# Performance work log

Hardware: AMD Instinct MI355X
Metric: run time of the kernel (lower is better)

Reference implementation:

```python
import math
import jax, jax.numpy as jnp
import numpy as np

N = 512; E_EDGES = 16384; NODE_DIM = 64; HID = 128; FF = 2048; VOCAB = 50; L = 2; H = 8; SEQ = 100


def setup_inputs() -> dict:
    key = jax.random.key(0)
    ks = jax.random.split(key, 24)
    s = 0.02
    rn = lambda k, shape: jax.random.normal(k, shape, jnp.float32) * s
    return {
        "x": jax.random.normal(ks[0], (N, NODE_DIM), jnp.float32),
        "edge_index": jax.random.randint(ks[1], (2, E_EDGES), 0, N, dtype=jnp.int32),
        "gcn1_w": rn(ks[2], (NODE_DIM, HID)), "gcn1_b": rn(ks[3], (HID,)),
        "gcn2_w": rn(ks[4], (HID, HID)),     "gcn2_b": rn(ks[5], (HID,)),
        "fc_w":   rn(ks[6], (HID, HID)),     "fc_b":   rn(ks[7], (HID,)),
        # decoder: per layer, 4 proj mats (q,k,v,out) for self-attn and cross-attn
        "sa_w": rn(ks[8], (L, 4, HID, HID)), "sa_b": rn(ks[9], (L, 4, HID)),
        "ca_w": rn(ks[10], (L, 4, HID, HID)), "ca_b": rn(ks[11], (L, 4, HID)),
        "ln_w": jnp.ones((L, 3, HID), jnp.float32), "ln_b": jnp.zeros((L, 3, HID), jnp.float32),
        "ff_w1": rn(ks[12], (L, HID, FF)), "ff_b1": rn(ks[13], (L, FF)),
        "ff_w2": rn(ks[14], (L, FF, HID)), "ff_b2": rn(ks[15], (L, HID)),
        "out_w": rn(ks[16], (HID, VOCAB)), "out_b": rn(ks[17], (VOCAB,)),
    }


def _gcn(x, W, b, src, dst, n):
    # PyG GCNConv: add self-loops, symmetric norm, aggregate source->target
    h = x @ W                                   # [N, out]
    loop = jnp.arange(n, dtype=src.dtype)
    s = jnp.concatenate([src, loop])
    d = jnp.concatenate([dst, loop])
    deg = jax.ops.segment_sum(jnp.ones_like(d, x.dtype), d, num_segments=n)
    dinv = jax.lax.rsqrt(deg)                   # deg >= 1 thanks to self-loops
    norm = dinv[s] * dinv[d]                    # [E+N]
    return jax.ops.segment_sum(h[s] * norm[:, None], d, num_segments=n) + b


def _layernorm(x, w, b, eps=1e-5):
    m = x.mean(-1, keepdims=True)
    v = ((x - m) ** 2).mean(-1, keepdims=True)
    return (x - m) * jax.lax.rsqrt(v + eps) * w + b


def _mha(q_in, kv_in, w, b):
    # q_in [S,Nb,E], kv_in [T,Nb,E]; w [4,E,E] (q,k,v,out), b [4,E]
    S, Nb, E = q_in.shape
    T = kv_in.shape[0]
    Dh = E // H
    q = (q_in @ w[0] + b[0]).reshape(S, Nb, H, Dh)
    k = (kv_in @ w[1] + b[1]).reshape(T, Nb, H, Dh)
    v = (kv_in @ w[2] + b[2]).reshape(T, Nb, H, Dh)
    att = jnp.einsum('snhd,tnhd->nhst', q, k) / math.sqrt(Dh)
    p = jax.nn.softmax(att, axis=-1)
    o = jnp.einsum('nhst,tnhd->snhd', p, v).reshape(S, Nb, E)
    return o @ w[3] + b[3]


def _forward(x, edge_index, gcn1_w, gcn1_b, gcn2_w, gcn2_b, fc_w, fc_b,
             sa_w, sa_b, ca_w, ca_b, ln_w, ln_b, ff_w1, ff_b1, ff_w2, ff_b2,
             out_w, out_b):
    n = x.shape[0]
    src, dst = edge_index[0], edge_index[1]
    # quantum_embedding: rz = (cos(phi)-sin(phi)) * (cos(theta)*x + sin(theta)*tanh(x))
    qx = (math.cos(0.05) - math.sin(0.05)) * (math.cos(0.1) * x + math.sin(0.1) * jnp.tanh(x))
    h = jax.nn.relu(_gcn(qx, gcn1_w, gcn1_b, src, dst, n))
    h = jax.nn.relu(_gcn(h, gcn2_w, gcn2_b, src, dst, n))
    h = h @ fc_w + fc_b                          # [N, HID]
    mem = h[None]                                # [1, N, HID] (memory, seq-first)
    tgt = jnp.zeros((SEQ, n, h.shape[1]), h.dtype)
    for l in range(L):                           # post-norm TransformerDecoderLayer
        tgt = _layernorm(tgt + _mha(tgt, tgt, sa_w[l], sa_b[l]), ln_w[l, 0], ln_b[l, 0])
        tgt = _layernorm(tgt + _mha(tgt, mem, ca_w[l], ca_b[l]), ln_w[l, 1], ln_b[l, 1])
        f = jax.nn.relu(tgt @ ff_w1[l] + ff_b1[l]) @ ff_w2[l] + ff_b2[l]
        tgt = _layernorm(tgt + f, ln_w[l, 2], ln_b[l, 2])
    return tgt @ out_w + out_b                   # [SEQ, N, VOCAB]


def reference(x, edge_index, gcn1_w, gcn1_b, gcn2_w, gcn2_b, fc_w, fc_b,
              sa_w, sa_b, ca_w, ca_b, ln_w, ln_b, ff_w1, ff_b1, ff_w2, ff_b2,
              out_w, out_b):
    return _forward(x, edge_index, gcn1_w, gcn1_b, gcn2_w, gcn2_b, fc_w, fc_b,
                    sa_w, sa_b, ca_w, ca_b, ln_w, ln_b, ff_w1, ff_b1, ff_w2, ff_b2,
                    out_w, out_b)
```

## Files before the change

### kernel.cpp

```cpp
#include <hip/hip_runtime.h>
#include <math.h>

#define NN      512
#define EE      16384
#define NDIM    64
#define HID     128
#define FFD     2048
#define VOCAB   50
#define SEQ     100

#define QA 0.94877109112428797f
#define QB 0.99500416527802582f
#define QC 0.099833416646828155f


__global__ void k_prep(const float* __restrict__ x, float* __restrict__ qx,
                       int* __restrict__ cnt) {
    int i = blockIdx.x * 256 + threadIdx.x;
    if (i < NN * NDIM) {
        float v = x[i];
        qx[i] = QA * (QB * v + QC * tanhf(v));
    }
    if (i < NN) cnt[i] = 0;
}


struct BArgs {
    const int* ei; int* cnt;
    const float* qx; const float* g1w; float* pre1;
    const float* A[3]; const float* ab[3]; const float* Bm[3]; const float* bb[3];
    float* outM[3];
    const float* ab3; const float* B3; const float* bb3; float* out3;
};

__global__ void k_b(BArgs a) {
    int B = blockIdx.x, t = threadIdx.x;
    if (B < 64) {
        int e = B * 256 + t;
        atomicAdd(&a.cnt[a.ei[EE + e]], 1);
        return;
    }
    if (B < 320) {
        int i = (B - 64) * 256 + t;
        int row = i >> 7, col = i & 127;
        const float* xr = a.qx + row * NDIM;
        float acc = 0.0f;
#pragma unroll 8
        for (int k = 0; k < NDIM; k++) acc = fmaf(xr[k], a.g1w[k * HID + col], acc);
        a.pre1[i] = acc;
        return;
    }
    if (B < 320 + 195) {
        int q = B - 320;
        int jm = q / 65;
        int i = (q - jm * 65) * 256 + t;
        if (i >= 129 * HID) return;
        int rw = i >> 7, col = i & 127;
        const float* Bm = a.Bm[jm];
        float acc;
        if (rw < 128) {
            const float* ar = a.A[jm] + rw * HID;
            acc = 0.0f;
#pragma unroll 8
            for (int k = 0; k < HID; k++) acc = fmaf(ar[k], Bm[k * HID + col], acc);
        } else {
            acc = a.bb[jm][col];
#pragma unroll 8
            for (int k = 0; k < HID; k++) acc = fmaf(a.ab[jm][k], Bm[k * HID + col], acc);
        }
        a.outM[jm][i] = acc;
        return;
    }
    if (t < HID) {
        float acc = a.bb3[t];
#pragma unroll 8
        for (int k = 0; k < HID; k++) acc = fmaf(a.ab3[k], a.B3[k * HID + t], acc);
        a.out3[t] = acc;
    }
}


struct CArgs {
    const int* cnt; int* offs; int* cursor; float* dinv;
    const float* fcw; const float* fcb;
    const float* Mca0; const float* Mca1; float* Mfc0; float* Mfc1;
};

__global__ void k_c(CArgs a) {
    int B = blockIdx.x, t = threadIdx.x;
    if (B == 0) {
        __shared__ int sh[512];
        int c0 = a.cnt[t], c1 = a.cnt[t + 256];
        sh[t] = c0; sh[t + 256] = c1;
        __syncthreads();
        for (int o = 1; o < 512; o <<= 1) {
            int x0 = (t >= o) ? sh[t - o] : 0;
            int x1 = (t + 256 >= o) ? sh[t + 256 - o] : 0;
            __syncthreads();
            sh[t] += x0; sh[t + 256] += x1;
            __syncthreads();
        }
        a.offs[t + 1] = sh[t];
        a.offs[t + 257] = sh[t + 256];
        if (t == 0) a.offs[0] = 0;
        a.cursor[t] = sh[t] - c0;
        a.cursor[t + 256] = sh[t + 256] - c1;
        a.dinv[t] = rsqrtf((float)c0 + 1.0f);
        a.dinv[t + 256] = rsqrtf((float)c1 + 1.0f);
        return;
    }
    int q = B - 1;
    int jm = q / 65;
    int i = (q - jm * 65) * 256 + t;
    if (i >= 129 * HID) return;
    int rw = i >> 7, col = i & 127;
    const float* M = jm ? a.Mca1 : a.Mca0;
    float* o = jm ? a.Mfc1 : a.Mfc0;
    float acc;
    if (rw < 128) {
        const float* ar = a.fcw + rw * HID;
        acc = 0.0f;
#pragma unroll 8
        for (int k = 0; k < HID; k++) acc = fmaf(ar[k], M[k * HID + col], acc);
    } else {
        acc = M[128 * HID + col];
#pragma unroll 8
        for (int k = 0; k < HID; k++) acc = fmaf(a.fcb[k], M[k * HID + col], acc);
    }
    o[i] = acc;
}


__global__ void k_scatter(const int* __restrict__ ei, int* __restrict__ cursor,
                          int* __restrict__ csr) {
    int e = blockIdx.x * 256 + threadIdx.x;
    if (e < EE) {
        int d = ei[EE + e];
        int slot = atomicAdd(&cursor[d], 1);
        csr[slot] = ei[e];
    }
}


__device__ __forceinline__ float gather_row(const float* __restrict__ pre,
                                            const float* __restrict__ dinv,
                                            const int* __restrict__ offs,
                                            const int* __restrict__ csr,
                                            int row, int j) {
    float dd = dinv[row];
    float acc = pre[row * HID + j] * dd;
    int i = offs[row], e = offs[row + 1];
    for (; i + 3 < e; i += 4) {
        int s0 = csr[i], s1 = csr[i + 1], s2 = csr[i + 2], s3 = csr[i + 3];
        float a0 = pre[s0 * HID + j] * dinv[s0];
        float a1 = pre[s1 * HID + j] * dinv[s1];
        float a2 = pre[s2 * HID + j] * dinv[s2];
        float a3 = pre[s3 * HID + j] * dinv[s3];
        acc += (a0 + a1) + (a2 + a3);
    }
    for (; i < e; ++i) {
        int s = csr[i];
        acc += pre[s * HID + j] * dinv[s];
    }
    return acc * dd;
}

__device__ __forceinline__ float rowln(float v, float w, float b, float* sh, int t) {
    int r = t >> 7;
    float s1 = v, s2 = v * v;
#pragma unroll
    for (int o = 32; o > 0; o >>= 1) {
        s1 += __shfl_down(s1, o);
        s2 += __shfl_down(s2, o);
    }
    int wv = (t >> 6) & 1;
    if ((t & 63) == 0) { sh[r * 4 + wv] = s1; sh[r * 4 + 2 + wv] = s2; }
    __syncthreads();
    float mean = (sh[r * 4] + sh[r * 4 + 1]) * (1.0f / HID);
    float m2   = (sh[r * 4 + 2] + sh[r * 4 + 3]) * (1.0f / HID);
    float rstd = rsqrtf(m2 - mean * mean + 1e-5f);
    float out = (v - mean) * rstd * w + b;
    __syncthreads();
    return out;
}


__global__ void k_gather_mm(const float* __restrict__ pre1, const float* __restrict__ dinv,
                            const int* __restrict__ offs, const int* __restrict__ csr,
                            const float* __restrict__ g1b, const float* __restrict__ g2w,
                            float* __restrict__ pre2) {
    __shared__ float sh_h[2][HID];
    int t = threadIdx.x, j = t & 127, r = t >> 7;
    int row = blockIdx.x * 2 + r;
    float g = gather_row(pre1, dinv, offs, csr, row, j);
    sh_h[r][j] = fmaxf(g + g1b[j], 0.0f);
    __syncthreads();
    float acc = 0.0f;
#pragma unroll 8
    for (int k = 0; k < HID; k++) acc = fmaf(sh_h[r][k], g2w[k * HID + j], acc);
    pre2[row * HID + j] = acc;
}


__global__ void k_row0(const float* __restrict__ pre2, const float* __restrict__ dinv,
                       const int* __restrict__ offs, const int* __restrict__ csr,
                       const float* __restrict__ g2b,
                       const float* __restrict__ Mfc0, const float* __restrict__ Mfc1,
                       const float* __restrict__ sa0bias,
                       const float* __restrict__ ln0w, const float* __restrict__ ln0b,
                       const float* __restrict__ ln1w, const float* __restrict__ ln1b,
                       float* __restrict__ ca1out, float* __restrict__ t0out) {
    __shared__ float sh_h[2][HID];
    __shared__ float shln[8];
    int t = threadIdx.x, j = t & 127, r = t >> 7;
    int row = blockIdx.x * 2 + r;
    float g = gather_row(pre2, dinv, offs, csr, row, j);
    sh_h[r][j] = fmaxf(g + g2b[j], 0.0f);
    __syncthreads();
    float a0 = Mfc0[128 * HID + j], a1 = Mfc1[128 * HID + j];
#pragma unroll 4
    for (int k = 0; k < HID; k++) {
        float hk = sh_h[r][k];
        a0 = fmaf(hk, Mfc0[k * HID + j], a0);
        a1 = fmaf(hk, Mfc1[k * HID + j], a1);
    }
    ca1out[row * HID + j] = a1;
    float v = rowln(sa0bias[j], ln0w[j], ln0b[j], shln, t);
    v = rowln(v + a0, ln1w[j], ln1b[j], shln, t);
    t0out[row * HID + j] = v;
}


__global__ void k_fff(const float* __restrict__ tin, const float* __restrict__ W1,
                      const float* __restrict__ b1, const float* __restrict__ W2,
                      float* __restrict__ part) {
    __shared__ float sh_t[8][HID];
    __shared__ float sh_m[8][256];
    int t = threadIdx.x;
    int kc = blockIdx.x & 7, rg = blockIdx.x >> 3;
    int row0 = rg * 8, c0 = kc * 256;
#pragma unroll
    for (int q = 0; q < 4; q++) {
        int i = q * 256 + t;
        sh_t[i >> 7][i & 127] = tin[row0 * HID + i];
    }
    __syncthreads();
    float acc[8];
    float bias = b1[c0 + t];
#pragma unroll
    for (int r = 0; r < 8; r++) acc[r] = bias;
#pragma unroll 4
    for (int k = 0; k < HID; k++) {
        float w = W1[k * FFD + c0 + t];
#pragma unroll
        for (int r = 0; r < 8; r++) acc[r] = fmaf(sh_t[r][k], w, acc[r]);
    }
#pragma unroll
    for (int r = 0; r < 8; r++) sh_m[r][t] = fmaxf(acc[r], 0.0f);
    __syncthreads();
    int col = t & 127, rr0 = (t >> 7) * 4;
    float a2[4] = {0.f, 0.f, 0.f, 0.f};
#pragma unroll 4
    for (int kk = 0; kk < 256; kk++) {
        float w = W2[(c0 + kk) * HID + col];
#pragma unroll
        for (int q = 0; q < 4; q++) a2[q] = fmaf(sh_m[rr0 + q][kk], w, a2[q]);
    }
#pragma unroll
    for (int q = 0; q < 4; q++)
        part[kc * (NN * HID) + (row0 + rr0 + q) * HID + col] = a2[q];
}


__global__ void k_row1(const float* __restrict__ part, const float* __restrict__ fb2,
                       const float* __restrict__ t0, const float* __restrict__ Msa1,
                       const float* __restrict__ ca1,
                       const float* __restrict__ ln2w, const float* __restrict__ ln2b,
                       const float* __restrict__ ln3w, const float* __restrict__ ln3b,
                       const float* __restrict__ ln4w, const float* __restrict__ ln4b,
                       float* __restrict__ t2out) {
    __shared__ float sh_t1[2][HID];
    __shared__ float shln[8];
    int t = threadIdx.x, j = t & 127, r = t >> 7;
    int row = blockIdx.x * 2 + r;
    float v = fb2[j] + t0[row * HID + j];
#pragma unroll
    for (int s = 0; s < 8; s++) v += part[s * (NN * HID) + row * HID + j];
    v = rowln(v, ln2w[j], ln2b[j], shln, t);
    sh_t1[r][j] = v;
    __syncthreads();
    float s1 = Msa1[128 * HID + j];
#pragma unroll 8
    for (int k = 0; k < HID; k++) s1 = fmaf(sh_t1[r][k], Msa1[k * HID + j], s1);
    float u = rowln(v + s1, ln3w[j], ln3b[j], shln, t);
    u = rowln(u + ca1[row * HID + j], ln4w[j], ln4b[j], shln, t);
    t2out[row * HID + j] = u;
}


__global__ void k_rowout(const float* __restrict__ part, const float* __restrict__ fb2,
                         const float* __restrict__ t2,
                         const float* __restrict__ ln5w, const float* __restrict__ ln5b,
                         const float* __restrict__ ow, const float* __restrict__ ob,
                         float* __restrict__ out) {
    __shared__ float sh3[2][HID];
    __shared__ float shln[8];
    __shared__ float sh_lg[100];
    int t = threadIdx.x, j = t & 127, r = t >> 7;
    int row = blockIdx.x * 2 + r;
    float v = fb2[j] + t2[row * HID + j];
#pragma unroll
    for (int s = 0; s < 8; s++) v += part[s * (NN * HID) + row * HID + j];
    v = rowln(v, ln5w[j], ln5b[j], shln, t);
    sh3[r][j] = v;
    __syncthreads();
    if (j < VOCAB) {
        float acc = ob[j];
#pragma unroll 8
        for (int k = 0; k < HID; k++) acc = fmaf(sh3[r][k], ow[k * VOCAB + j], acc);
        sh_lg[r * VOCAB + j] = acc;
    }
    __syncthreads();
    int base = blockIdx.x * (2 * VOCAB);
    for (int idx = t; idx < SEQ * 2 * VOCAB; idx += 256) {
        int s = idx / (2 * VOCAB), p = idx - s * (2 * VOCAB);
        out[s * (NN * VOCAB) + base + p] = sh_lg[p];
    }
}


extern "C" void kernel_launch(void* const* d_in, const int* in_sizes, int n_in,
                              void* d_out, int out_size, void* d_ws, size_t ws_size,
                              hipStream_t stream) {
    (void)in_sizes; (void)n_in; (void)out_size; (void)ws_size;
    const float* x   = (const float*)d_in[0];
    const int*   ei  = (const int*)d_in[1];
    const float* g1w = (const float*)d_in[2];
    const float* g1b = (const float*)d_in[3];
    const float* g2w = (const float*)d_in[4];
    const float* g2b = (const float*)d_in[5];
    const float* fcw = (const float*)d_in[6];
    const float* fcb = (const float*)d_in[7];
    const float* saw = (const float*)d_in[8];
    const float* sab = (const float*)d_in[9];
    const float* caw = (const float*)d_in[10];
    const float* cab = (const float*)d_in[11];
    const float* lnw = (const float*)d_in[12];
    const float* lnb = (const float*)d_in[13];
    const float* fw1 = (const float*)d_in[14];
    const float* fb1 = (const float*)d_in[15];
    const float* fw2 = (const float*)d_in[16];
    const float* fb2 = (const float*)d_in[17];
    const float* ow  = (const float*)d_in[18];
    const float* ob  = (const float*)d_in[19];
    float* out = (float*)d_out;

    float* ws      = (float*)d_ws;
    float* qx      = ws;
    float* pre1    = ws + 32768;
    float* pre2    = ws + 98304;
    float* t0      = ws + 163840;
    float* t2      = ws + 229376;
    float* ca1     = ws + 294912;
    float* Msa1    = ws + 360448;
    float* Mca0    = ws + 376960;
    float* Mca1    = ws + 393472;
    float* Mfc0    = ws + 409984;
    float* Mfc1    = ws + 426496;
    float* sa0bias = ws + 443008;
    float* dinv    = ws + 443136;
    int*   cnt     = (int*)(ws + 443648);
    int*   offs    = cnt + 512;
    int*   cursor  = offs + 516;
    int*   csr     = cursor + 512;
    float* part    = ws + 461824;

    k_prep<<<128, 256, 0, stream>>>(x, qx, cnt);

    {
        BArgs a;
        a.ei = ei; a.cnt = cnt; a.qx = qx; a.g1w = g1w; a.pre1 = pre1;
        a.A[0]  = saw + (4 + 2) * HID * HID;  a.ab[0] = sab + (4 + 2) * HID;
        a.Bm[0] = saw + (4 + 3) * HID * HID;  a.bb[0] = sab + (4 + 3) * HID;
        a.outM[0] = Msa1;
        a.A[1]  = caw + 2 * HID * HID;        a.ab[1] = cab + 2 * HID;
        a.Bm[1] = caw + 3 * HID * HID;        a.bb[1] = cab + 3 * HID;
        a.outM[1] = Mca0;
        a.A[2]  = caw + (4 + 2) * HID * HID;  a.ab[2] = cab + (4 + 2) * HID;
        a.Bm[2] = caw + (4 + 3) * HID * HID;  a.bb[2] = cab + (4 + 3) * HID;
        a.outM[2] = Mca1;
        a.ab3 = sab + 2 * HID;  a.B3 = saw + 3 * HID * HID;  a.bb3 = sab + 3 * HID;
        a.out3 = sa0bias;
        k_b<<<516, 256, 0, stream>>>(a);
    }

    {
        CArgs a;
        a.cnt = cnt; a.offs = offs; a.cursor = cursor; a.dinv = dinv;
        a.fcw = fcw; a.fcb = fcb;
        a.Mca0 = Mca0; a.Mca1 = Mca1; a.Mfc0 = Mfc0; a.Mfc1 = Mfc1;
        k_c<<<131, 256, 0, stream>>>(a);
    }

    k_scatter<<<64, 256, 0, stream>>>(ei, cursor, csr);

    k_gather_mm<<<256, 256, 0, stream>>>(pre1, dinv, offs, csr, g1b, g2w, pre2);

    k_row0<<<256, 256, 0, stream>>>(pre2, dinv, offs, csr, g2b, Mfc0, Mfc1, sa0bias,
                                    lnw + 0 * HID, lnb + 0 * HID,
                                    lnw + 1 * HID, lnb + 1 * HID, ca1, t0);

    k_fff<<<512, 256, 0, stream>>>(t0, fw1, fb1, fw2, part);

    k_row1<<<256, 256, 0, stream>>>(part, fb2, t0, Msa1, ca1,
                                    lnw + 2 * HID, lnb + 2 * HID,
                                    lnw + 3 * HID, lnb + 3 * HID,
                                    lnw + 4 * HID, lnb + 4 * HID, t2);

    k_fff<<<512, 256, 0, stream>>>(t2, fw1 + HID * FFD, fb1 + FFD, fw2 + FFD * HID, part);

    k_rowout<<<256, 256, 0, stream>>>(part, fb2 + HID, t2,
                                      lnw + 5 * HID, lnb + 5 * HID, ow, ob, out);
}
```

Measured before the change: 113.4 us.

## Prefetch FFN weights into cache in k_b and vectorize k_fff with 512 threads

Adds 512 extra blocks to k_b that read the FFN weight matrices fw1/fw2 and write a dummy reduction, so the weights are warm in L2/MALL by the time k_fff runs. k_fff is rewritten to use 512 threads with float4 weight loads, each thread computing 4 columns per row. The second GEMM is split over two halves of K and reduced through shared memory. This costs extra traffic and blocks in k_b and a dummy workspace output, plus an added shared-memory reduction step.

```diff
diff --git a/kernel.cpp b/kernel.cpp
--- a/kernel.cpp
+++ b/kernel.cpp
@@ -31,6 +31,7 @@
     const float* A[3]; const float* ab[3]; const float* Bm[3]; const float* bb[3];
     float* outM[3];
     const float* ab3; const float* B3; const float* bb3; float* out3;
+    const float* fw1; const float* fw2; float* pf;
 };
 
 __global__ void k_b(BArgs a) {
@@ -71,11 +72,25 @@
         a.outM[jm][i] = acc;
         return;
     }
-    if (t < HID) {
-        float acc = a.bb3[t];
-#pragma unroll 8
-        for (int k = 0; k < HID; k++) acc = fmaf(a.ab3[k], a.B3[k * HID + t], acc);
-        a.out3[t] = acc;
+    if (B == 515) {
+        if (t < HID) {
+            float acc = a.bb3[t];
+#pragma unroll 8
+            for (int k = 0; k < HID; k++) acc = fmaf(a.ab3[k], a.B3[k * HID + t], acc);
+            a.out3[t] = acc;
+        }
+        return;
+    }
+    {
+        int q = B - 516;
+        const float4* p = (const float4*)((q < 256) ? (a.fw1 + q * 2048)
+                                                    : (a.fw2 + (q - 256) * 2048));
+        float4 f0 = p[t];
+        float4 f1 = p[t + 256];
+        float s = (f0.x + f0.y + f0.z + f0.w) + (f1.x + f1.y + f1.z + f1.w);
+#pragma unroll
+        for (int o = 32; o > 0; o >>= 1) s += __shfl_down(s, o);
+        if ((t & 63) == 0) a.pf[q * 4 + (t >> 6)] = s;
     }
 }
 
@@ -231,44 +246,71 @@
 }
 
 
-__global__ void k_fff(const float* __restrict__ tin, const float* __restrict__ W1,
-                      const float* __restrict__ b1, const float* __restrict__ W2,
-                      float* __restrict__ part) {
+__global__ __launch_bounds__(512, 4)
+void k_fff(const float* __restrict__ tin, const float* __restrict__ W1,
+           const float* __restrict__ b1, const float* __restrict__ W2,
+           float* __restrict__ part) {
     __shared__ float sh_t[8][HID];
     __shared__ float sh_m[8][256];
     int t = threadIdx.x;
     int kc = blockIdx.x & 7, rg = blockIdx.x >> 3;
     int row0 = rg * 8, c0 = kc * 256;
-#pragma unroll
-    for (int q = 0; q < 4; q++) {
-        int i = q * 256 + t;
-        sh_t[i >> 7][i & 127] = tin[row0 * HID + i];
-    }
-    __syncthreads();
-    float acc[8];
-    float bias = b1[c0 + t];
-#pragma unroll
-    for (int r = 0; r < 8; r++) acc[r] = bias;
-#pragma unroll 4
-    for (int k = 0; k < HID; k++) {
-        float w = W1[k * FFD + c0 + t];
-#pragma unroll
-        for (int r = 0; r < 8; r++) acc[r] = fmaf(sh_t[r][k], w, acc[r]);
-    }
-#pragma unroll
-    for (int r = 0; r < 8; r++) sh_m[r][t] = fmaxf(acc[r], 0.0f);
-    __syncthreads();
-    int col = t & 127, rr0 = (t >> 7) * 4;
-    float a2[4] = {0.f, 0.f, 0.f, 0.f};
-#pragma unroll 4
-    for (int kk = 0; kk < 256; kk++) {
-        float w = W2[(c0 + kk) * HID + col];
-#pragma unroll
-        for (int q = 0; q < 4; q++) a2[q] = fmaf(sh_m[rr0 + q][kk], w, a2[q]);
-    }
-#pragma unroll
-    for (int q = 0; q < 4; q++)
-        part[kc * (NN * HID) + (row0 + rr0 + q) * HID + col] = a2[q];
+
+    if (t < 256) {
+        const float4* tp = (const float4*)(tin + row0 * HID);
+        float4 v = tp[t];
+        *(float4*)&sh_t[t >> 5][(t & 31) * 4] = v;
+    }
+    __syncthreads();
+
+    {
+        int rowg = t >> 6;
+        int col4 = (t & 63) * 4;
+        float4 bias = *(const float4*)&b1[c0 + col4];
+        float a0 = bias.x, a1 = bias.y, a2 = bias.z, a3 = bias.w;
+        const float* w1p = W1 + c0 + col4;
+#pragma unroll 8
+        for (int k = 0; k < HID; k++) {
+            float4 w = *(const float4*)&w1p[k * FFD];
+            float s = sh_t[rowg][k];
+            a0 = fmaf(s, w.x, a0); a1 = fmaf(s, w.y, a1);
+            a2 = fmaf(s, w.z, a2); a3 = fmaf(s, w.w, a3);
+        }
+        float4 m;
+        m.x = fmaxf(a0, 0.f); m.y = fmaxf(a1, 0.f);
+        m.z = fmaxf(a2, 0.f); m.w = fmaxf(a3, 0.f);
+        *(float4*)&sh_m[rowg][col4] = m;
+    }
+    __syncthreads();
+
+    {
+        int col4 = (t & 31) * 4;
+        int rowg = (t >> 5) & 7;
+        int half = t >> 8;
+        int kb = half * 128;
+        float a0 = 0.f, a1 = 0.f, a2 = 0.f, a3 = 0.f;
+        const float* w2p = W2 + (c0 + kb) * HID + col4;
+        const float* mp = &sh_m[rowg][kb];
+#pragma unroll 8
+        for (int kk = 0; kk < 128; kk++) {
+            float4 w = *(const float4*)&w2p[kk * HID];
+            float m = mp[kk];
+            a0 = fmaf(m, w.x, a0); a1 = fmaf(m, w.y, a1);
+            a2 = fmaf(m, w.z, a2); a3 = fmaf(m, w.w, a3);
+        }
+        __syncthreads();
+        float* shred = &sh_t[0][0];
+        if (half) {
+            float4 r; r.x = a0; r.y = a1; r.z = a2; r.w = a3;
+            *(float4*)&shred[(t - 256) * 4] = r;
+        }
+        __syncthreads();
+        if (!half) {
+            float4 o = *(float4*)&shred[t * 4];
+            o.x += a0; o.y += a1; o.z += a2; o.w += a3;
+            *(float4*)&part[kc * (NN * HID) + (row0 + rowg) * HID + col4] = o;
+        }
+    }
 }
 
 
@@ -374,6 +416,7 @@
     int*   cursor  = offs + 516;
     int*   csr     = cursor + 512;
     float* part    = ws + 461824;
+    float* pf      = ws + 986112;
 
     k_prep<<<128, 256, 0, stream>>>(x, qx, cnt);
 
@@ -391,7 +434,8 @@
         a.outM[2] = Mca1;
         a.ab3 = sab + 2 * HID;  a.B3 = saw + 3 * HID * HID;  a.bb3 = sab + 3 * HID;
         a.out3 = sa0bias;
-        k_b<<<516, 256, 0, stream>>>(a);
+        a.fw1 = fw1; a.fw2 = fw2; a.pf = pf;
+        k_b<<<1028, 256, 0, stream>>>(a);
     }
 
     {
@@ -410,14 +454,14 @@
                                     lnw + 0 * HID, lnb + 0 * HID,
                                     lnw + 1 * HID, lnb + 1 * HID, ca1, t0);
 
-    k_fff<<<512, 256, 0, stream>>>(t0, fw1, fb1, fw2, part);
+    k_fff<<<512, 512, 0, stream>>>(t0, fw1, fb1, fw2, part);
 
     k_row1<<<256, 256, 0, stream>>>(part, fb2, t0, Msa1, ca1,
                                     lnw + 2 * HID, lnb + 2 * HID,
                                     lnw + 3 * HID, lnb + 3 * HID,
                                     lnw + 4 * HID, lnb + 4 * HID, t2);
 
-    k_fff<<<512, 256, 0, stream>>>(t2, fw1 + HID * FFD, fb1 + FFD, fw2 + FFD * HID, part);
+    k_fff<<<512, 512, 0, stream>>>(t2, fw1 + HID * FFD, fb1 + FFD, fw2 + FFD * HID, part);
 
     k_rowout<<<256, 256, 0, stream>>>(part, fb2 + HID, t2,
                                       lnw + 5 * HID, lnb + 5 * HID, ow, ob, out);
```

Measured after the change: 135.0 us. 19.1% more time.

## Fuse input prep into GEMM, retile FFN to 16 rows with float4 loads

Applied to the files above, without the earlier changes.

The separate prep kernel goes away: the tanh transform is computed in shared memory inside the first GEMM branch, and the count buffer is cleared with a memset. The FFN kernel now handles 16 rows per block with 512 threads and register-blocked float4 weight loads, which doubles weight reuse per fetch. The output broadcast writes float4 stores. These changes aim to cut one launch, global weight traffic and store instruction count, at the cost of more registers and shared memory per block.

```diff
diff --git a/kernel.cpp b/kernel.cpp
--- a/kernel.cpp
+++ b/kernel.cpp
@@ -14,20 +14,9 @@
 #define QC 0.099833416646828155f
 
 
-__global__ void k_prep(const float* __restrict__ x, float* __restrict__ qx,
-                       int* __restrict__ cnt) {
-    int i = blockIdx.x * 256 + threadIdx.x;
-    if (i < NN * NDIM) {
-        float v = x[i];
-        qx[i] = QA * (QB * v + QC * tanhf(v));
-    }
-    if (i < NN) cnt[i] = 0;
-}
-
-
 struct BArgs {
     const int* ei; int* cnt;
-    const float* qx; const float* g1w; float* pre1;
+    const float* x; const float* g1w; float* pre1;
     const float* A[3]; const float* ab[3]; const float* Bm[3]; const float* bb[3];
     float* outM[3];
     const float* ab3; const float* B3; const float* bb3; float* out3;
@@ -41,13 +30,19 @@
         return;
     }
     if (B < 320) {
-        int i = (B - 64) * 256 + t;
-        int row = i >> 7, col = i & 127;
-        const float* xr = a.qx + row * NDIM;
+        __shared__ float qxs[2][NDIM];
+        int q = B - 64;
+        int row0 = q * 2;
+        if (t < 2 * NDIM) {
+            float v = a.x[row0 * NDIM + t];
+            qxs[t >> 6][t & 63] = QA * (QB * v + QC * tanhf(v));
+        }
+        __syncthreads();
+        int r = t >> 7, col = t & 127;
         float acc = 0.0f;
 #pragma unroll 8
-        for (int k = 0; k < NDIM; k++) acc = fmaf(xr[k], a.g1w[k * HID + col], acc);
-        a.pre1[i] = acc;
+        for (int k = 0; k < NDIM; k++) acc = fmaf(qxs[r][k], a.g1w[k * HID + col], acc);
+        a.pre1[(row0 + r) * HID + col] = acc;
         return;
     }
     if (B < 320 + 195) {
@@ -231,44 +226,67 @@
 }
 
 
-__global__ void k_fff(const float* __restrict__ tin, const float* __restrict__ W1,
-                      const float* __restrict__ b1, const float* __restrict__ W2,
-                      float* __restrict__ part) {
-    __shared__ float sh_t[8][HID];
-    __shared__ float sh_m[8][256];
+__global__ __launch_bounds__(512)
+void k_fff(const float* __restrict__ tin, const float* __restrict__ W1,
+           const float* __restrict__ b1, const float* __restrict__ W2,
+           float* __restrict__ part) {
+    __shared__ float sh_t[16][HID];
+    __shared__ float sh_m[16][256];
     int t = threadIdx.x;
     int kc = blockIdx.x & 7, rg = blockIdx.x >> 3;
-    int row0 = rg * 8, c0 = kc * 256;
-#pragma unroll
-    for (int q = 0; q < 4; q++) {
-        int i = q * 256 + t;
-        sh_t[i >> 7][i & 127] = tin[row0 * HID + i];
-    }
-    __syncthreads();
-    float acc[8];
-    float bias = b1[c0 + t];
-#pragma unroll
-    for (int r = 0; r < 8; r++) acc[r] = bias;
-#pragma unroll 4
-    for (int k = 0; k < HID; k++) {
-        float w = W1[k * FFD + c0 + t];
-#pragma unroll
-        for (int r = 0; r < 8; r++) acc[r] = fmaf(sh_t[r][k], w, acc[r]);
-    }
-#pragma unroll
-    for (int r = 0; r < 8; r++) sh_m[r][t] = fmaxf(acc[r], 0.0f);
-    __syncthreads();
-    int col = t & 127, rr0 = (t >> 7) * 4;
-    float a2[4] = {0.f, 0.f, 0.f, 0.f};
-#pragma unroll 4
-    for (int kk = 0; kk < 256; kk++) {
-        float w = W2[(c0 + kk) * HID + col];
-#pragma unroll
-        for (int q = 0; q < 4; q++) a2[q] = fmaf(sh_m[rr0 + q][kk], w, a2[q]);
-    }
-#pragma unroll
-    for (int q = 0; q < 4; q++)
-        part[kc * (NN * HID) + (row0 + rr0 + q) * HID + col] = a2[q];
+    int row0 = rg * 16, c0 = kc * 256;
+
+    {
+        const float4* tp = (const float4*)(tin + row0 * HID);
+        float4 v = tp[t];
+        *(float4*)&sh_t[t >> 5][(t & 31) * 4] = v;
+    }
+    __syncthreads();
+
+    {
+        int rg2  = t >> 6;
+        int col4 = (t & 63) * 4;
+        float4 bias = *(const float4*)&b1[c0 + col4];
+        float a00 = bias.x, a01 = bias.y, a02 = bias.z, a03 = bias.w;
+        float a10 = bias.x, a11 = bias.y, a12 = bias.z, a13 = bias.w;
+        const float* w1p = W1 + c0 + col4;
+        const float* x0 = sh_t[2 * rg2];
+        const float* x1 = sh_t[2 * rg2 + 1];
+#pragma unroll 8
+        for (int k = 0; k < HID; k++) {
+            float4 w = *(const float4*)&w1p[k * FFD];
+            float s0 = x0[k], s1 = x1[k];
+            a00 = fmaf(s0, w.x, a00); a01 = fmaf(s0, w.y, a01);
+            a02 = fmaf(s0, w.z, a02); a03 = fmaf(s0, w.w, a03);
+            a10 = fmaf(s1, w.x, a10); a11 = fmaf(s1, w.y, a11);
+            a12 = fmaf(s1, w.z, a12); a13 = fmaf(s1, w.w, a13);
+        }
+        float4 m0, m1;
+        m0.x = fmaxf(a00, 0.f); m0.y = fmaxf(a01, 0.f);
+        m0.z = fmaxf(a02, 0.f); m0.w = fmaxf(a03, 0.f);
+        m1.x = fmaxf(a10, 0.f); m1.y = fmaxf(a11, 0.f);
+        m1.z = fmaxf(a12, 0.f); m1.w = fmaxf(a13, 0.f);
+        *(float4*)&sh_m[2 * rg2][col4]     = m0;
+        *(float4*)&sh_m[2 * rg2 + 1][col4] = m1;
+    }
+    __syncthreads();
+
+    {
+        int rowg = t >> 5;
+        int col4 = (t & 31) * 4;
+        float a0 = 0.f, a1 = 0.f, a2 = 0.f, a3 = 0.f;
+        const float* w2p = W2 + c0 * HID + col4;
+        const float* mp = sh_m[rowg];
+#pragma unroll 8
+        for (int kk = 0; kk < 256; kk++) {
+            float4 w = *(const float4*)&w2p[kk * HID];
+            float m = mp[kk];
+            a0 = fmaf(m, w.x, a0); a1 = fmaf(m, w.y, a1);
+            a2 = fmaf(m, w.z, a2); a3 = fmaf(m, w.w, a3);
+        }
+        float4 o; o.x = a0; o.y = a1; o.z = a2; o.w = a3;
+        *(float4*)&part[kc * (NN * HID) + (row0 + rowg) * HID + col4] = o;
+    }
 }
 
 
@@ -305,7 +323,7 @@
                          float* __restrict__ out) {
     __shared__ float sh3[2][HID];
     __shared__ float shln[8];
-    __shared__ float sh_lg[100];
+    __shared__ __align__(16) float sh_lg[100];
     int t = threadIdx.x, j = t & 127, r = t >> 7;
     int row = blockIdx.x * 2 + r;
     float v = fb2[j] + t2[row * HID + j];
@@ -322,9 +340,9 @@
     }
     __syncthreads();
     int base = blockIdx.x * (2 * VOCAB);
-    for (int idx = t; idx < SEQ * 2 * VOCAB; idx += 256) {
-        int s = idx / (2 * VOCAB), p = idx - s * (2 * VOCAB);
-        out[s * (NN * VOCAB) + base + p] = sh_lg[p];
+    for (int idx = t; idx < SEQ * 25; idx += 256) {
+        int s = idx / 25, p4 = (idx - s * 25) * 4;
+        *(float4*)&out[s * (NN * VOCAB) + base + p4] = *(const float4*)&sh_lg[p4];
     }
 }
 
@@ -356,30 +374,29 @@
     float* out = (float*)d_out;
 
     float* ws      = (float*)d_ws;
-    float* qx      = ws;
-    float* pre1    = ws + 32768;
-    float* pre2    = ws + 98304;
-    float* t0      = ws + 163840;
-    float* t2      = ws + 229376;
-    float* ca1     = ws + 294912;
-    float* Msa1    = ws + 360448;
-    float* Mca0    = ws + 376960;
-    float* Mca1    = ws + 393472;
-    float* Mfc0    = ws + 409984;
-    float* Mfc1    = ws + 426496;
-    float* sa0bias = ws + 443008;
-    float* dinv    = ws + 443136;
-    int*   cnt     = (int*)(ws + 443648);
+    float* pre1    = ws;
+    float* pre2    = ws + 65536;
+    float* t0      = ws + 131072;
+    float* t2      = ws + 196608;
+    float* ca1     = ws + 262144;
+    float* Msa1    = ws + 327680;
+    float* Mca0    = ws + 344192;
+    float* Mca1    = ws + 360704;
+    float* Mfc0    = ws + 377216;
+    float* Mfc1    = ws + 393728;
+    float* sa0bias = ws + 410240;
+    float* dinv    = ws + 410368;
+    int*   cnt     = (int*)(ws + 410880);
     int*   offs    = cnt + 512;
     int*   cursor  = offs + 516;
     int*   csr     = cursor + 512;
-    float* part    = ws + 461824;
-
-    k_prep<<<128, 256, 0, stream>>>(x, qx, cnt);
+    float* part    = ws + 429056;
+
+    hipMemsetAsync(cnt, 0, 512 * sizeof(int), stream);
 
     {
         BArgs a;
-        a.ei = ei; a.cnt = cnt; a.qx = qx; a.g1w = g1w; a.pre1 = pre1;
+        a.ei = ei; a.cnt = cnt; a.x = x; a.g1w = g1w; a.pre1 = pre1;
         a.A[0]  = saw + (4 + 2) * HID * HID;  a.ab[0] = sab + (4 + 2) * HID;
         a.Bm[0] = saw + (4 + 3) * HID * HID;  a.bb[0] = sab + (4 + 3) * HID;
         a.outM[0] = Msa1;
@@ -410,14 +427,14 @@
                                     lnw + 0 * HID, lnb + 0 * HID,
                                     lnw + 1 * HID, lnb + 1 * HID, ca1, t0);
 
-    k_fff<<<512, 256, 0, stream>>>(t0, fw1, fb1, fw2, part);
+    k_fff<<<256, 512, 0, stream>>>(t0, fw1, fb1, fw2, part);
 
     k_row1<<<256, 256, 0, stream>>>(part, fb2, t0, Msa1, ca1,
                                     lnw + 2 * HID, lnb + 2 * HID,
                                     lnw + 3 * HID, lnb + 3 * HID,
                                     lnw + 4 * HID, lnb + 4 * HID, t2);
 
-    k_fff<<<512, 256, 0, stream>>>(t2, fw1 + HID * FFD, fb1 + FFD, fw2 + FFD * HID, part);
+    k_fff<<<256, 512, 0, stream>>>(t2, fw1 + HID * FFD, fb1 + FFD, fw2 + FFD * HID, part);
 
     k_rowout<<<256, 256, 0, stream>>>(part, fb2 + HID, t2,
                                       lnw + 5 * HID, lnb + 5 * HID, ow, ob, out);
```

Result: slower. 120.2 us (+6.0%).
